# Optimization experiments

Measured on AMD Instinct MI355X. Metric: run time of the kernel, lower is better.

## Reference

```python
import jax, jax.numpy as jnp
import numpy as np

NUM_ITEMS = 50000
NUM_USERS = 16384   # static number of user segments (total_user universe)
H0 = 512            # encoder_hidden_size[0]
LAT = 256           # bottleneck (encoder_hidden_size[-1] / decoder_hidden_size[0])
N = 262144          # observed interactions
NT = 262144         # target interactions


def setup_inputs() -> dict:
    key = jax.random.key(0)
    ks = jax.random.split(key, 14)

    def glorot(k, shape):
        fan_in, fan_out = shape[1], shape[0]
        lim = np.sqrt(6.0 / (fan_in + fan_out)).astype(np.float32)
        return jax.random.uniform(k, shape, jnp.float32, -lim, lim)

    return {
        "user": jax.random.randint(ks[0], (N,), 0, NUM_USERS, jnp.int32),
        "item": jax.random.randint(ks[1], (N,), 0, NUM_ITEMS, jnp.int32),
        "rating": jax.random.normal(ks[2], (N,), jnp.float32),
        "target_user": jax.random.randint(ks[3], (NT,), 0, NUM_USERS, jnp.int32),
        "target_item": jax.random.randint(ks[4], (NT,), 0, NUM_ITEMS, jnp.int32),
        "target_rating": jax.random.normal(ks[5], (NT,), jnp.float32),
        # encoder_linear: Linear(num_items, H0)
        "W_enc": glorot(ks[6], (H0, NUM_ITEMS)),
        "b_enc": jnp.zeros((H0,), jnp.float32),
        # Encoder: Linear(H0, LAT) + Tanh
        "W1": glorot(ks[7], (LAT, H0)),
        "b1": jnp.zeros((LAT,), jnp.float32),
        # Decoder: Linear(LAT, H0) + Tanh
        "W2": glorot(ks[8], (H0, LAT)),
        "b2": jnp.zeros((H0,), jnp.float32),
        # decoder_linear: Linear(H0, num_items)
        "W_dec": glorot(ks[9], (NUM_ITEMS, H0)),
        "b_dec": jnp.zeros((NUM_ITEMS,), jnp.float32),
    }


def reference(user, item, rating, target_user, target_item, target_rating,
              W_enc, b_enc, W1, b1, W2, b2, W_dec, b_dec):
    # --- encoder: gather item weight rows, scale by rating, segment-sum per user ---
    # rows: [N, H0] gather from W_enc.T ([NUM_ITEMS, H0])
    rows = W_enc.T[item] * rating[:, None]
    # per-user aggregation over the full user universe (equivalent to the
    # torch unique/sort/index_add path: users with no interactions get 0 -> tanh(bias))
    agg = jax.ops.segment_sum(rows, user, num_segments=NUM_USERS)  # [U, H0]
    x = jnp.tanh(agg + b_enc)
    # --- small dense tanh MLP encoder/decoder ---
    encoded = jnp.tanh(x @ W1.T + b1)          # [U, LAT]
    decoded = jnp.tanh(encoded @ W2.T + b2)    # [U, H0] (dropout = identity, eval mode)
    # --- decoder: gather user codes & item decoder rows, rowwise dot ---
    g = decoded[target_user]                   # [NT, H0]
    w = W_dec[target_item]                     # [NT, H0]
    pred = jnp.sum(g * w, axis=-1) + b_dec[target_item]  # [NT]
    loss = jnp.mean((pred - target_rating) ** 2)
    return pred, loss
```

## Files before the change

kernel.cpp:

```cpp
#include <hip/hip_runtime.h>
#include <hip/hip_bf16.h>
#include <math.h>

#define NUM_ITEMS 50000
#define NUM_USERS 16384
#define ITEM_BINS 65536
#define H0 512
#define LAT 256
#define FP8_SCALE 64.0f
#define FP8_INV (1.0f / 64.0f)

typedef __attribute__((ext_vector_type(8))) short short8;
typedef __attribute__((ext_vector_type(4))) float floatx4;
typedef __attribute__((ext_vector_type(2))) float vf2;

__device__ __forceinline__ unsigned short f2bf(float f) {
    union { float f; unsigned i; } u; u.f = f;
    unsigned r = u.i + 0x7fff + ((u.i >> 16) & 1);
    return (unsigned short)(r >> 16);
}
__device__ __forceinline__ float bfhi(unsigned v) {
    union { unsigned i; float f; } u; u.i = v & 0xffff0000u; return u.f;
}
__device__ __forceinline__ float bflo(unsigned v) {
    union { unsigned i; float f; } u; u.i = v << 16; return u.f;
}
__device__ __forceinline__ uint4 pack8(const float* v) {
    uint4 p;
    p.x = (unsigned)f2bf(v[0]) | ((unsigned)f2bf(v[1]) << 16);
    p.y = (unsigned)f2bf(v[2]) | ((unsigned)f2bf(v[3]) << 16);
    p.z = (unsigned)f2bf(v[4]) | ((unsigned)f2bf(v[5]) << 16);
    p.w = (unsigned)f2bf(v[6]) | ((unsigned)f2bf(v[7]) << 16);
    return p;
}
__device__ __forceinline__ unsigned pkfp8_4(float a, float b, float c, float d) {
    int v = __builtin_amdgcn_cvt_pk_fp8_f32(a, b, 0, false);
    v = __builtin_amdgcn_cvt_pk_fp8_f32(c, d, v, true);
    return (unsigned)v;
}
__device__ __forceinline__ void fp8x4_to_f32(unsigned v, float* o) {
    vf2 lo = __builtin_amdgcn_cvt_pk_f32_fp8((int)v, false);
    vf2 hi = __builtin_amdgcn_cvt_pk_f32_fp8((int)v, true);
    o[0] = lo.x; o[1] = lo.y; o[2] = hi.x; o[3] = hi.y;
}

__global__ __launch_bounds__(256) void count_kernel(const int* __restrict__ user, int* __restrict__ cntU,
                                                    const int* __restrict__ t_item, int* __restrict__ cntI,
                                                    int n, int nt) {
    int i = (blockIdx.x * blockDim.x + threadIdx.x) * 4;
    if (i + 3 < n) {
        int4 u = *(const int4*)(user + i);
        atomicAdd(&cntU[u.x], 1); atomicAdd(&cntU[u.y], 1);
        atomicAdd(&cntU[u.z], 1); atomicAdd(&cntU[u.w], 1);
    } else {
        for (int k = i; k < n; ++k) atomicAdd(&cntU[user[k]], 1);
    }
    if (i + 3 < nt) {
        int4 t = *(const int4*)(t_item + i);
        atomicAdd(&cntI[t.x], 1); atomicAdd(&cntI[t.y], 1);
        atomicAdd(&cntI[t.z], 1); atomicAdd(&cntI[t.w], 1);
    } else {
        for (int k = i; k < nt; ++k) atomicAdd(&cntI[t_item[k]], 1);
    }
}

__device__ void scan_block(const int* __restrict__ cnt, int* __restrict__ offs,
                           int* __restrict__ cursor, int per) {
    __shared__ int ssum[1024];
    int t = threadIdx.x;
    int base = t * per;
    int s = 0;
    for (int j = 0; j < per; j += 4) {
        int4 v = *(const int4*)(cnt + base + j);
        s += v.x + v.y + v.z + v.w;
    }
    ssum[t] = s;
    __syncthreads();
    for (int off = 1; off < 1024; off <<= 1) {
        int v = (t >= off) ? ssum[t - off] : 0;
        __syncthreads();
        ssum[t] += v;
        __syncthreads();
    }
    int run = (t == 0) ? 0 : ssum[t - 1];
    for (int j = 0; j < per; j += 4) {
        int4 v = *(const int4*)(cnt + base + j);
        int4 o;
        o.x = run; run += v.x;
        o.y = run; run += v.y;
        o.z = run; run += v.z;
        o.w = run; run += v.w;
        *(int4*)(offs + base + j) = o;
        *(int4*)(cursor + base + j) = o;
    }
}

__global__ void scan_kernel(const int* __restrict__ cntU, int* __restrict__ offsU, int* __restrict__ curU,
                            const int* __restrict__ cntI, int* __restrict__ offsI, int* __restrict__ curI) {
    if (blockIdx.x == 0) scan_block(cntU, offsU, curU, NUM_USERS / 1024);
    else scan_block(cntI, offsI, curI, ITEM_BINS / 1024);
}

__global__ __launch_bounds__(256) void mega_kernel(
        const int* __restrict__ user, const int* __restrict__ item,
        const float* __restrict__ rating, int* __restrict__ curU, int2* __restrict__ s_pack,
        const int* __restrict__ t_user, const int* __restrict__ t_item,
        const float* __restrict__ t_rating, int* __restrict__ curI, int4* __restrict__ st_pack,
        const float* __restrict__ W_enc, unsigned char* __restrict__ wtb8,
        const float* __restrict__ W_dec, unsigned char* __restrict__ wdb8,
        const float* __restrict__ W1, unsigned short* __restrict__ w1b,
        const float* __restrict__ W2, unsigned short* __restrict__ w2b,
        int n, int nt, int SB, int TB, int DB) {
    __shared__ float tileT[64 * 129];
    int bid = blockIdx.x;
    int tid = threadIdx.x;
    if (bid < SB) {
        int i = bid * 256 + tid;
        if (i < n) {
            int u = user[i];
            int pos = atomicAdd(&curU[u], 1);
            s_pack[pos] = make_int2(item[i], __float_as_int(rating[i]));
        }
        if (i < nt) {
            int it = t_item[i];
            int pos = atomicAdd(&curI[it], 1);
            st_pack[pos] = make_int4(t_user[i], it, __float_as_int(t_rating[i]), i);
        }
    } else if (bid < SB + TB) {
        const int TBX = (NUM_ITEMS + 63) / 64;
        int b = bid - SB;
        int x0 = (b % TBX) * 64;
        int y0 = (b / TBX) * 128;
        int g = tid >> 4;
        int m = tid & 15;
        int ibase = m * 4;
#pragma unroll
        for (int p = 0; p < 8; ++p) {
            int hloc = p * 16 + g;
            int it = x0 + ibase;
            if (it < NUM_ITEMS) {
                float4 v = *(const float4*)(W_enc + (size_t)(y0 + hloc) * NUM_ITEMS + it);
                tileT[(ibase + 0) * 129 + hloc] = v.x;
                tileT[(ibase + 1) * 129 + hloc] = v.y;
                tileT[(ibase + 2) * 129 + hloc] = v.z;
                tileT[(ibase + 3) * 129 + hloc] = v.w;
            }
        }
        __syncthreads();
        int l = tid & 7;
        int i0 = tid >> 3;
#pragma unroll
        for (int p = 0; p < 2; ++p) {
            int i = p * 32 + i0;
            int it = x0 + i;
            if (it < NUM_ITEMS) {
                const float* src = tileT + i * 129 + l * 16;
                uint4 o;
                o.x = pkfp8_4(src[0] * FP8_SCALE, src[1] * FP8_SCALE, src[2] * FP8_SCALE, src[3] * FP8_SCALE);
                o.y = pkfp8_4(src[4] * FP8_SCALE, src[5] * FP8_SCALE, src[6] * FP8_SCALE, src[7] * FP8_SCALE);
                o.z = pkfp8_4(src[8] * FP8_SCALE, src[9] * FP8_SCALE, src[10] * FP8_SCALE, src[11] * FP8_SCALE);
                o.w = pkfp8_4(src[12] * FP8_SCALE, src[13] * FP8_SCALE, src[14] * FP8_SCALE, src[15] * FP8_SCALE);
                *(uint4*)(wtb8 + (size_t)it * H0 + y0 + l * 16) = o;
            }
        }
    } else if (bid < SB + TB + DB) {
        size_t idx = (size_t)(bid - SB - TB) * 4096 + tid * 16;
        float4 v0 = *(const float4*)(W_dec + idx);
        float4 v1 = *(const float4*)(W_dec + idx + 4);
        float4 v2 = *(const float4*)(W_dec + idx + 8);
        float4 v3 = *(const float4*)(W_dec + idx + 12);
        uint4 o;
        o.x = pkfp8_4(v0.x * FP8_SCALE, v0.y * FP8_SCALE, v0.z * FP8_SCALE, v0.w * FP8_SCALE);
        o.y = pkfp8_4(v1.x * FP8_SCALE, v1.y * FP8_SCALE, v1.z * FP8_SCALE, v1.w * FP8_SCALE);
        o.z = pkfp8_4(v2.x * FP8_SCALE, v2.y * FP8_SCALE, v2.z * FP8_SCALE, v2.w * FP8_SCALE);
        o.w = pkfp8_4(v3.x * FP8_SCALE, v3.y * FP8_SCALE, v3.z * FP8_SCALE, v3.w * FP8_SCALE);
        *(uint4*)(wdb8 + idx) = o;
    } else {
        int b2i = bid - SB - TB - DB;
        const float* src = (b2i < 64) ? W1 : W2;
        unsigned short* dst = (b2i < 64) ? w1b : w2b;
        int idx = (b2i & 63) * 2048 + tid * 8;
        float v[8];
        *(float4*)&v[0] = *(const float4*)(src + idx);
        *(float4*)&v[4] = *(const float4*)(src + idx + 4);
        *(uint4*)(dst + idx) = pack8(v);
    }
}

__global__ __launch_bounds__(256) void agg_kernel(const unsigned char* __restrict__ wtb8,
                                                  const int* __restrict__ offs,
                                                  const int* __restrict__ ends,
                                                  const int2* __restrict__ s_pack,
                                                  const float* __restrict__ b_enc,
                                                  unsigned short* __restrict__ xb) {
    __shared__ float red[3 * 512];
    int u = blockIdx.x;
    int tid = threadIdx.x;
    int g = tid >> 6, lane = tid & 63;
    float acc[8] = {};
    int j0 = offs[u], j1 = ends[u];
    int j = j0 + g;
    int2 nxt = (j < j1) ? s_pack[j] : make_int2(0, 0);
    while (j < j1) {
        int2 cur = nxt;
        int jn = j + 4;
        if (jn < j1) nxt = s_pack[jn];
        float r = __int_as_float(cur.y);
        uint2 v = ((const uint2*)(wtb8 + (size_t)cur.x * H0))[lane];
        float wf[8];
        fp8x4_to_f32(v.x, wf);
        fp8x4_to_f32(v.y, wf + 4);
#pragma unroll
        for (int e = 0; e < 8; ++e) acc[e] += wf[e] * r;
        j = jn;
    }
    if (g) {
        float4* rp = (float4*)red + (size_t)(g - 1) * 128 + lane * 2;
        rp[0] = make_float4(acc[0], acc[1], acc[2], acc[3]);
        rp[1] = make_float4(acc[4], acc[5], acc[6], acc[7]);
    }
    __syncthreads();
    if (g == 0) {
#pragma unroll
        for (int h = 0; h < 3; ++h) {
            const float* rp = red + h * 512 + lane * 8;
#pragma unroll
            for (int e = 0; e < 8; ++e) acc[e] += rp[e];
        }
        float4 b0 = ((const float4*)b_enc)[lane * 2];
        float4 b1 = ((const float4*)b_enc)[lane * 2 + 1];
        float o[8];
        o[0] = tanhf(acc[0] * FP8_INV + b0.x); o[1] = tanhf(acc[1] * FP8_INV + b0.y);
        o[2] = tanhf(acc[2] * FP8_INV + b0.z); o[3] = tanhf(acc[3] * FP8_INV + b0.w);
        o[4] = tanhf(acc[4] * FP8_INV + b1.x); o[5] = tanhf(acc[5] * FP8_INV + b1.y);
        o[6] = tanhf(acc[6] * FP8_INV + b1.z); o[7] = tanhf(acc[7] * FP8_INV + b1.w);
        ((uint4*)(xb + (size_t)u * H0))[lane] = pack8(o);
    }
}

template<int BN>
__global__ __launch_bounds__(256) void gemm_mfma(const unsigned short* __restrict__ A,
                                                 const unsigned short* __restrict__ B,
                                                 const float* __restrict__ bias,
                                                 unsigned short* __restrict__ C,
                                                 int Nn, int K) {
    constexpr int WN = BN / 32;
    constexpr int NCH = 8 + BN / 16;
    constexpr int PER = NCH / 4;
    __shared__ unsigned short Ash[128 * 32];
    __shared__ unsigned short Bsh[BN * 32];
    int tid = threadIdx.x;
    int wid = tid >> 6, lane = tid & 63;
    int wave_m = wid & 1, wave_n = wid >> 1;
    int quad = lane >> 4, l16 = lane & 15;
    int m0 = blockIdx.x * 128, n0 = blockIdx.y * BN;
    floatx4 acc[4][WN] = {};
    int srow = lane >> 2;
    int scol = (lane & 3) * 8;
    for (int k0 = 0; k0 < K; k0 += 32) {
#pragma unroll
        for (int i = 0; i < PER; ++i) {
            int c = wid * PER + i;
            if (c < 8) {
                const unsigned short* ga = A + (size_t)(m0 + c * 16 + srow) * K + k0 + scol;
                __builtin_amdgcn_global_load_lds(
                    (const __attribute__((address_space(1))) void*)ga,
                    (__attribute__((address_space(3))) void*)((__attribute__((address_space(3))) char*)Ash + c * 1024),
                    16, 0, 0);
            } else {
                const unsigned short* gb = B + (size_t)(n0 + (c - 8) * 16 + srow) * K + k0 + scol;
                __builtin_amdgcn_global_load_lds(
                    (const __attribute__((address_space(1))) void*)gb,
                    (__attribute__((address_space(3))) void*)((__attribute__((address_space(3))) char*)Bsh + (c - 8) * 1024),
                    16, 0, 0);
            }
        }
        __syncthreads();
        short8 af[4], bfr[WN];
#pragma unroll
        for (int i = 0; i < 4; ++i) {
            int ml = wave_m * 64 + i * 16 + l16;
            af[i] = ((const short8*)Ash)[ml * 4 + quad];
        }
#pragma unroll
        for (int j = 0; j < WN; ++j) {
            int nl = wave_n * (BN / 2) + j * 16 + l16;
            bfr[j] = ((const short8*)Bsh)[nl * 4 + quad];
        }
#pragma unroll
        for (int i = 0; i < 4; ++i)
#pragma unroll
            for (int j = 0; j < WN; ++j)
                acc[i][j] = __builtin_amdgcn_mfma_f32_16x16x32_bf16(af[i], bfr[j], acc[i][j], 0, 0, 0);
        __syncthreads();
    }
#pragma unroll
    for (int j = 0; j < WN; ++j) {
        int col = n0 + wave_n * (BN / 2) + j * 16 + l16;
        float bv = bias[col];
#pragma unroll
        for (int i = 0; i < 4; ++i) {
            int rowb = m0 + wave_m * 64 + i * 16 + quad * 4;
#pragma unroll
            for (int r = 0; r < 4; ++r)
                C[(size_t)(rowb + r) * Nn + col] = f2bf(tanhf(acc[i][j][r] + bv));
        }
    }
}

__global__ __launch_bounds__(256) void predict_kernel(const unsigned short* __restrict__ dec_b,
                                                      const unsigned char* __restrict__ wdb8,
                                                      const float* __restrict__ b_dec,
                                                      const int4* __restrict__ st,
                                                      float* __restrict__ pred,
                                                      float* __restrict__ partials, int NT) {
    __shared__ float wsum[4];
    int wid = threadIdx.x >> 6, lane = threadIdx.x & 63;
    int base = (blockIdx.x * 4 + wid) * 4;
    float sq = 0.f;
    int4 tv[4];
    uint4 gv[4];
    uint2 wv[4];
#pragma unroll
    for (int t = 0; t < 4; ++t) tv[t] = st[min(base + t, NT - 1)];
#pragma unroll
    for (int t = 0; t < 4; ++t) {
        gv[t] = ((const uint4*)(dec_b + (size_t)tv[t].x * H0))[lane];
        wv[t] = ((const uint2*)(wdb8 + (size_t)tv[t].y * H0))[lane];
    }
#pragma unroll
    for (int t = 0; t < 4; ++t) {
        float wf[8];
        fp8x4_to_f32(wv[t].x, wf);
        fp8x4_to_f32(wv[t].y, wf + 4);
        float s = bflo(gv[t].x) * wf[0] + bfhi(gv[t].x) * wf[1]
                + bflo(gv[t].y) * wf[2] + bfhi(gv[t].y) * wf[3]
                + bflo(gv[t].z) * wf[4] + bfhi(gv[t].z) * wf[5]
                + bflo(gv[t].w) * wf[6] + bfhi(gv[t].w) * wf[7];
#pragma unroll
        for (int off = 32; off; off >>= 1) s += __shfl_xor(s, off, 64);
        if (lane == 0 && base + t < NT) {
            float p = s * FP8_INV + b_dec[tv[t].y];
            pred[tv[t].w] = p;
            float d = p - __int_as_float(tv[t].z);
            sq += d * d;
        }
    }
    if (lane == 0) wsum[wid] = sq;
    __syncthreads();
    if (threadIdx.x == 0) partials[blockIdx.x] = wsum[0] + wsum[1] + wsum[2] + wsum[3];
}

__global__ void loss_reduce(const float* __restrict__ partials, float* __restrict__ out_loss,
                            int nPart, float invNT) {
    __shared__ float s[256];
    int t = threadIdx.x;
    float a = 0.f;
    const float4* p4 = (const float4*)partials;
    int n4 = nPart >> 2;
    for (int i = t; i < n4; i += 256) {
        float4 v = p4[i];
        a += v.x + v.y + v.z + v.w;
    }
    for (int i = (n4 << 2) + t; i < nPart; i += 256) a += partials[i];
    s[t] = a;
    __syncthreads();
    for (int off = 128; off; off >>= 1) {
        if (t < off) s[t] += s[t + off];
        __syncthreads();
    }
    if (t == 0) out_loss[0] = s[0] * invNT;
}

extern "C" void kernel_launch(void* const* d_in, const int* in_sizes, int n_in,
                              void* d_out, int out_size, void* d_ws, size_t ws_size,
                              hipStream_t stream) {
    const int* user = (const int*)d_in[0];
    const int* item = (const int*)d_in[1];
    const float* rating = (const float*)d_in[2];
    const int* t_user = (const int*)d_in[3];
    const int* t_item = (const int*)d_in[4];
    const float* t_rating = (const float*)d_in[5];
    const float* W_enc = (const float*)d_in[6];
    const float* b_enc = (const float*)d_in[7];
    const float* W1 = (const float*)d_in[8];
    const float* b1 = (const float*)d_in[9];
    const float* W2 = (const float*)d_in[10];
    const float* b2 = (const float*)d_in[11];
    const float* W_dec = (const float*)d_in[12];
    const float* b_dec = (const float*)d_in[13];
    const int N = in_sizes[0];
    const int NT = in_sizes[3];

    char* ws = (char*)d_ws;
    size_t off = 0;
    auto alloc = [&](size_t bytes) {
        void* p = ws + off;
        off = (off + bytes + 255) & ~(size_t)255;
        return p;
    };
    unsigned char* wtb8 = (unsigned char*)alloc((size_t)NUM_ITEMS * H0);
    unsigned char* wdb8 = (unsigned char*)alloc((size_t)NUM_ITEMS * H0);
    unsigned short* xb = (unsigned short*)alloc((size_t)NUM_USERS * H0 * 2);
    unsigned short* enc_b = (unsigned short*)alloc((size_t)NUM_USERS * LAT * 2);
    unsigned short* dec_b = (unsigned short*)alloc((size_t)NUM_USERS * H0 * 2);
    unsigned short* w1b = (unsigned short*)alloc((size_t)LAT * H0 * 2);
    unsigned short* w2b = (unsigned short*)alloc((size_t)H0 * LAT * 2);
    int* cntU = (int*)alloc((size_t)(NUM_USERS + ITEM_BINS) * 4);
    int* cntI = cntU + NUM_USERS;
    int* offsU = (int*)alloc((size_t)NUM_USERS * 4);
    int* curU = (int*)alloc((size_t)NUM_USERS * 4);
    int* offsI = (int*)alloc((size_t)ITEM_BINS * 4);
    int* curI = (int*)alloc((size_t)ITEM_BINS * 4);
    int2* s_pack = (int2*)alloc((size_t)N * 8);
    int4* st_pack = (int4*)alloc((size_t)NT * 16);
    const int predBlocks = (NT + 15) / 16;
    float* partials = (float*)alloc((size_t)predBlocks * 4);

    float* pred = (float*)d_out;
    float* loss = pred + NT;

    const int maxNNT = N > NT ? N : NT;
    const int SB = (maxNNT + 255) / 256;
    const int TBX = (NUM_ITEMS + 63) / 64;
    const int TB = TBX * (H0 / 128);
    const int DB = (NUM_ITEMS * H0) / 4096;
    const int WB = 128;

    hipMemsetAsync(cntU, 0, (size_t)(NUM_USERS + ITEM_BINS) * 4, stream);
    count_kernel<<<(maxNNT + 1023) / 1024, 256, 0, stream>>>(user, cntU, t_item, cntI, N, NT);
    scan_kernel<<<2, 1024, 0, stream>>>(cntU, offsU, curU, cntI, offsI, curI);
    mega_kernel<<<SB + TB + DB + WB, 256, 0, stream>>>(
        user, item, rating, curU, s_pack,
        t_user, t_item, t_rating, curI, st_pack,
        W_enc, wtb8, W_dec, wdb8, W1, w1b, W2, w2b,
        N, NT, SB, TB, DB);
    agg_kernel<<<NUM_USERS, 256, 0, stream>>>(wtb8, offsU, curU, s_pack, b_enc, xb);
    gemm_mfma<64><<<dim3(NUM_USERS / 128, LAT / 64), 256, 0, stream>>>(xb, w1b, b1, enc_b, LAT, H0);
    gemm_mfma<64><<<dim3(NUM_USERS / 128, H0 / 64), 256, 0, stream>>>(enc_b, w2b, b2, dec_b, H0, LAT);
    predict_kernel<<<predBlocks, 256, 0, stream>>>(dec_b, wdb8, b_dec, st_pack, pred, partials, NT);
    loss_reduce<<<1, 256, 0, stream>>>(partials, loss, predBlocks, 1.0f / NT);
}
```

Before: 450.9 us.

## Fuse encoder/decoder GEMMs, use one wave per user in aggregation, simplify conversions

```diff
diff --git a/kernel.cpp b/kernel.cpp
--- a/kernel.cpp
+++ b/kernel.cpp
@@ -9,6 +9,7 @@
 #define LAT 256
 #define FP8_SCALE 64.0f
 #define FP8_INV (1.0f / 64.0f)
+#define EPITCH 264
 
 typedef __attribute__((ext_vector_type(8))) short short8;
 typedef __attribute__((ext_vector_type(4))) float floatx4;
@@ -46,7 +47,8 @@
 
 __global__ __launch_bounds__(256) void count_kernel(const int* __restrict__ user, int* __restrict__ cntU,
                                                     const int* __restrict__ t_item, int* __restrict__ cntI,
-                                                    int n, int nt) {
+                                                    float* __restrict__ loss, int n, int nt) {
+    if (blockIdx.x == 0 && threadIdx.x == 0) loss[0] = 0.f;
     int i = (blockIdx.x * blockDim.x + threadIdx.x) * 4;
     if (i + 3 < n) {
         int4 u = *(const int4*)(user + i);
@@ -111,9 +113,9 @@
         const float* __restrict__ W1, unsigned short* __restrict__ w1b,
         const float* __restrict__ W2, unsigned short* __restrict__ w2b,
         int n, int nt, int SB, int TB, int DB) {
-    __shared__ float tileT[64 * 129];
     int bid = blockIdx.x;
     int tid = threadIdx.x;
+    int wid = tid >> 6, lane = tid & 63;
     if (bid < SB) {
         int i = bid * 256 + tid;
         if (i < n) {
@@ -130,60 +132,42 @@
         const int TBX = (NUM_ITEMS + 63) / 64;
         int b = bid - SB;
         int x0 = (b % TBX) * 64;
-        int y0 = (b / TBX) * 128;
-        int g = tid >> 4;
-        int m = tid & 15;
-        int ibase = m * 4;
-#pragma unroll
-        for (int p = 0; p < 8; ++p) {
-            int hloc = p * 16 + g;
-            int it = x0 + ibase;
-            if (it < NUM_ITEMS) {
-                float4 v = *(const float4*)(W_enc + (size_t)(y0 + hloc) * NUM_ITEMS + it);
-                tileT[(ibase + 0) * 129 + hloc] = v.x;
-                tileT[(ibase + 1) * 129 + hloc] = v.y;
-                tileT[(ibase + 2) * 129 + hloc] = v.z;
-                tileT[(ibase + 3) * 129 + hloc] = v.w;
-            }
-        }
-        __syncthreads();
-        int l = tid & 7;
-        int i0 = tid >> 3;
-#pragma unroll
-        for (int p = 0; p < 2; ++p) {
-            int i = p * 32 + i0;
-            int it = x0 + i;
-            if (it < NUM_ITEMS) {
-                const float* src = tileT + i * 129 + l * 16;
-                uint4 o;
-                o.x = pkfp8_4(src[0] * FP8_SCALE, src[1] * FP8_SCALE, src[2] * FP8_SCALE, src[3] * FP8_SCALE);
-                o.y = pkfp8_4(src[4] * FP8_SCALE, src[5] * FP8_SCALE, src[6] * FP8_SCALE, src[7] * FP8_SCALE);
-                o.z = pkfp8_4(src[8] * FP8_SCALE, src[9] * FP8_SCALE, src[10] * FP8_SCALE, src[11] * FP8_SCALE);
-                o.w = pkfp8_4(src[12] * FP8_SCALE, src[13] * FP8_SCALE, src[14] * FP8_SCALE, src[15] * FP8_SCALE);
-                *(uint4*)(wtb8 + (size_t)it * H0 + y0 + l * 16) = o;
-            }
+        int y0 = (b / TBX) * 64;
+        int h0 = y0 + wid * 16;
+        int it = x0 + lane;
+        if (it < NUM_ITEMS) {
+            float v[16];
+#pragma unroll
+            for (int e = 0; e < 16; ++e)
+                v[e] = W_enc[(size_t)(h0 + e) * NUM_ITEMS + it];
+            uint4 o;
+            o.x = pkfp8_4(v[0] * FP8_SCALE, v[1] * FP8_SCALE, v[2] * FP8_SCALE, v[3] * FP8_SCALE);
+            o.y = pkfp8_4(v[4] * FP8_SCALE, v[5] * FP8_SCALE, v[6] * FP8_SCALE, v[7] * FP8_SCALE);
+            o.z = pkfp8_4(v[8] * FP8_SCALE, v[9] * FP8_SCALE, v[10] * FP8_SCALE, v[11] * FP8_SCALE);
+            o.w = pkfp8_4(v[12] * FP8_SCALE, v[13] * FP8_SCALE, v[14] * FP8_SCALE, v[15] * FP8_SCALE);
+            *(uint4*)(wtb8 + (size_t)it * H0 + h0) = o;
         }
     } else if (bid < SB + TB + DB) {
-        size_t idx = (size_t)(bid - SB - TB) * 4096 + tid * 16;
-        float4 v0 = *(const float4*)(W_dec + idx);
-        float4 v1 = *(const float4*)(W_dec + idx + 4);
-        float4 v2 = *(const float4*)(W_dec + idx + 8);
-        float4 v3 = *(const float4*)(W_dec + idx + 12);
-        uint4 o;
-        o.x = pkfp8_4(v0.x * FP8_SCALE, v0.y * FP8_SCALE, v0.z * FP8_SCALE, v0.w * FP8_SCALE);
-        o.y = pkfp8_4(v1.x * FP8_SCALE, v1.y * FP8_SCALE, v1.z * FP8_SCALE, v1.w * FP8_SCALE);
-        o.z = pkfp8_4(v2.x * FP8_SCALE, v2.y * FP8_SCALE, v2.z * FP8_SCALE, v2.w * FP8_SCALE);
-        o.w = pkfp8_4(v3.x * FP8_SCALE, v3.y * FP8_SCALE, v3.z * FP8_SCALE, v3.w * FP8_SCALE);
-        *(uint4*)(wdb8 + idx) = o;
+        size_t base = (size_t)(bid - SB - TB) * 4096 + wid * 1024 + lane * 4;
+#pragma unroll
+        for (int c = 0; c < 4; ++c) {
+            float4 v = *(const float4*)(W_dec + base + c * 256);
+            *(unsigned*)(wdb8 + base + c * 256) =
+                pkfp8_4(v.x * FP8_SCALE, v.y * FP8_SCALE, v.z * FP8_SCALE, v.w * FP8_SCALE);
+        }
     } else {
         int b2i = bid - SB - TB - DB;
-        const float* src = (b2i < 64) ? W1 : W2;
-        unsigned short* dst = (b2i < 64) ? w1b : w2b;
-        int idx = (b2i & 63) * 2048 + tid * 8;
-        float v[8];
-        *(float4*)&v[0] = *(const float4*)(src + idx);
-        *(float4*)&v[4] = *(const float4*)(src + idx + 4);
-        *(uint4*)(dst + idx) = pack8(v);
+        const float* src = (b2i < 32) ? W1 : W2;
+        unsigned short* dst = (b2i < 32) ? w1b : w2b;
+        size_t base = (size_t)(b2i & 31) * 4096 + wid * 1024 + lane * 4;
+#pragma unroll
+        for (int c = 0; c < 4; ++c) {
+            float4 v = *(const float4*)(src + base + c * 256);
+            uint2 o;
+            o.x = (unsigned)f2bf(v.x) | ((unsigned)f2bf(v.y) << 16);
+            o.y = (unsigned)f2bf(v.z) | ((unsigned)f2bf(v.w) << 16);
+            *(uint2*)(dst + base + c * 256) = o;
+        }
     }
 }
 
@@ -193,117 +177,148 @@
                                                   const int2* __restrict__ s_pack,
                                                   const float* __restrict__ b_enc,
                                                   unsigned short* __restrict__ xb) {
-    __shared__ float red[3 * 512];
-    int u = blockIdx.x;
-    int tid = threadIdx.x;
-    int g = tid >> 6, lane = tid & 63;
+    int wid = threadIdx.x >> 6, lane = threadIdx.x & 63;
+    int u = blockIdx.x * 4 + wid;
+    int j0 = offs[u], j1 = ends[u];
     float acc[8] = {};
-    int j0 = offs[u], j1 = ends[u];
-    int j = j0 + g;
-    int2 nxt = (j < j1) ? s_pack[j] : make_int2(0, 0);
-    while (j < j1) {
-        int2 cur = nxt;
-        int jn = j + 4;
-        if (jn < j1) nxt = s_pack[jn];
-        float r = __int_as_float(cur.y);
-        uint2 v = ((const uint2*)(wtb8 + (size_t)cur.x * H0))[lane];
-        float wf[8];
-        fp8x4_to_f32(v.x, wf);
-        fp8x4_to_f32(v.y, wf + 4);
-#pragma unroll
-        for (int e = 0; e < 8; ++e) acc[e] += wf[e] * r;
-        j = jn;
-    }
-    if (g) {
-        float4* rp = (float4*)red + (size_t)(g - 1) * 128 + lane * 2;
-        rp[0] = make_float4(acc[0], acc[1], acc[2], acc[3]);
-        rp[1] = make_float4(acc[4], acc[5], acc[6], acc[7]);
-    }
-    __syncthreads();
-    if (g == 0) {
-#pragma unroll
-        for (int h = 0; h < 3; ++h) {
-            const float* rp = red + h * 512 + lane * 8;
-#pragma unroll
-            for (int e = 0; e < 8; ++e) acc[e] += rp[e];
-        }
-        float4 b0 = ((const float4*)b_enc)[lane * 2];
-        float4 b1 = ((const float4*)b_enc)[lane * 2 + 1];
-        float o[8];
-        o[0] = tanhf(acc[0] * FP8_INV + b0.x); o[1] = tanhf(acc[1] * FP8_INV + b0.y);
-        o[2] = tanhf(acc[2] * FP8_INV + b0.z); o[3] = tanhf(acc[3] * FP8_INV + b0.w);
-        o[4] = tanhf(acc[4] * FP8_INV + b1.x); o[5] = tanhf(acc[5] * FP8_INV + b1.y);
-        o[6] = tanhf(acc[6] * FP8_INV + b1.z); o[7] = tanhf(acc[7] * FP8_INV + b1.w);
-        ((uint4*)(xb + (size_t)u * H0))[lane] = pack8(o);
-    }
-}
-
-template<int BN>
-__global__ __launch_bounds__(256) void gemm_mfma(const unsigned short* __restrict__ A,
-                                                 const unsigned short* __restrict__ B,
-                                                 const float* __restrict__ bias,
-                                                 unsigned short* __restrict__ C,
-                                                 int Nn, int K) {
-    constexpr int WN = BN / 32;
-    constexpr int NCH = 8 + BN / 16;
-    constexpr int PER = NCH / 4;
-    __shared__ unsigned short Ash[128 * 32];
-    __shared__ unsigned short Bsh[BN * 32];
+    int j = j0;
+    for (; j + 1 < j1; j += 2) {
+        int2 a = s_pack[j];
+        int2 b = s_pack[j + 1];
+        uint2 va = ((const uint2*)(wtb8 + (size_t)a.x * H0))[lane];
+        uint2 vb = ((const uint2*)(wtb8 + (size_t)b.x * H0))[lane];
+        float ra = __int_as_float(a.y), rb = __int_as_float(b.y);
+        float wa[8], wb[8];
+        fp8x4_to_f32(va.x, wa); fp8x4_to_f32(va.y, wa + 4);
+        fp8x4_to_f32(vb.x, wb); fp8x4_to_f32(vb.y, wb + 4);
+#pragma unroll
+        for (int e = 0; e < 8; ++e) acc[e] += wa[e] * ra + wb[e] * rb;
+    }
+    if (j < j1) {
+        int2 a = s_pack[j];
+        uint2 va = ((const uint2*)(wtb8 + (size_t)a.x * H0))[lane];
+        float ra = __int_as_float(a.y);
+        float wa[8];
+        fp8x4_to_f32(va.x, wa); fp8x4_to_f32(va.y, wa + 4);
+#pragma unroll
+        for (int e = 0; e < 8; ++e) acc[e] += wa[e] * ra;
+    }
+    float4 b0 = ((const float4*)b_enc)[lane * 2];
+    float4 b1 = ((const float4*)b_enc)[lane * 2 + 1];
+    float o[8];
+    o[0] = tanhf(acc[0] * FP8_INV + b0.x); o[1] = tanhf(acc[1] * FP8_INV + b0.y);
+    o[2] = tanhf(acc[2] * FP8_INV + b0.z); o[3] = tanhf(acc[3] * FP8_INV + b0.w);
+    o[4] = tanhf(acc[4] * FP8_INV + b1.x); o[5] = tanhf(acc[5] * FP8_INV + b1.y);
+    o[6] = tanhf(acc[6] * FP8_INV + b1.z); o[7] = tanhf(acc[7] * FP8_INV + b1.w);
+    ((uint4*)(xb + (size_t)u * H0))[lane] = pack8(o);
+}
+
+__global__ __launch_bounds__(256) void mlp_kernel(const unsigned short* __restrict__ xb,
+                                                  const unsigned short* __restrict__ w1b,
+                                                  const float* __restrict__ b1,
+                                                  const unsigned short* __restrict__ w2b,
+                                                  const float* __restrict__ b2,
+                                                  unsigned short* __restrict__ dec_b) {
+    __shared__ unsigned short Ash[64 * 32];
+    __shared__ unsigned short Bsh[512 * 32];
+    __shared__ unsigned short encs[64 * EPITCH];
     int tid = threadIdx.x;
     int wid = tid >> 6, lane = tid & 63;
-    int wave_m = wid & 1, wave_n = wid >> 1;
     int quad = lane >> 4, l16 = lane & 15;
-    int m0 = blockIdx.x * 128, n0 = blockIdx.y * BN;
-    floatx4 acc[4][WN] = {};
+    int m0 = blockIdx.x * 64;
     int srow = lane >> 2;
     int scol = (lane & 3) * 8;
-    for (int k0 = 0; k0 < K; k0 += 32) {
-#pragma unroll
-        for (int i = 0; i < PER; ++i) {
-            int c = wid * PER + i;
-            if (c < 8) {
-                const unsigned short* ga = A + (size_t)(m0 + c * 16 + srow) * K + k0 + scol;
-                __builtin_amdgcn_global_load_lds(
-                    (const __attribute__((address_space(1))) void*)ga,
-                    (__attribute__((address_space(3))) void*)((__attribute__((address_space(3))) char*)Ash + c * 1024),
-                    16, 0, 0);
-            } else {
-                const unsigned short* gb = B + (size_t)(n0 + (c - 8) * 16 + srow) * K + k0 + scol;
-                __builtin_amdgcn_global_load_lds(
-                    (const __attribute__((address_space(1))) void*)gb,
-                    (__attribute__((address_space(3))) void*)((__attribute__((address_space(3))) char*)Bsh + (c - 8) * 1024),
-                    16, 0, 0);
+
+    {
+        floatx4 acc[4][4] = {};
+        for (int k0 = 0; k0 < 512; k0 += 32) {
+#pragma unroll
+            for (int i = 0; i < 5; ++i) {
+                int c = wid * 5 + i;
+                if (c < 4) {
+                    const unsigned short* ga = xb + (size_t)(m0 + c * 16 + srow) * 512 + k0 + scol;
+                    __builtin_amdgcn_global_load_lds(
+                        (const __attribute__((address_space(1))) void*)ga,
+                        (__attribute__((address_space(3))) void*)((__attribute__((address_space(3))) char*)Ash + c * 1024),
+                        16, 0, 0);
+                } else {
+                    const unsigned short* gb = w1b + (size_t)((c - 4) * 16 + srow) * 512 + k0 + scol;
+                    __builtin_amdgcn_global_load_lds(
+                        (const __attribute__((address_space(1))) void*)gb,
+                        (__attribute__((address_space(3))) void*)((__attribute__((address_space(3))) char*)Bsh + (c - 4) * 1024),
+                        16, 0, 0);
+                }
             }
+            __syncthreads();
+            short8 af[4], bfr[4];
+#pragma unroll
+            for (int i = 0; i < 4; ++i)
+                af[i] = ((const short8*)Ash)[(i * 16 + l16) * 4 + quad];
+#pragma unroll
+            for (int j = 0; j < 4; ++j) {
+                int nl = wid * 64 + j * 16 + l16;
+                bfr[j] = ((const short8*)Bsh)[nl * 4 + quad];
+            }
+#pragma unroll
+            for (int i = 0; i < 4; ++i)
+#pragma unroll
+                for (int j = 0; j < 4; ++j)
+                    acc[i][j] = __builtin_amdgcn_mfma_f32_16x16x32_bf16(af[i], bfr[j], acc[i][j], 0, 0, 0);
+            __syncthreads();
+        }
+#pragma unroll
+        for (int j = 0; j < 4; ++j) {
+            int col = wid * 64 + j * 16 + l16;
+            float bv = b1[col];
+#pragma unroll
+            for (int i = 0; i < 4; ++i) {
+                int row = i * 16 + quad * 4;
+#pragma unroll
+                for (int r = 0; r < 4; ++r)
+                    encs[(row + r) * EPITCH + col] = f2bf(tanhf(acc[i][j][r] + bv));
+            }
+        }
+    }
+    __syncthreads();
+
+    floatx4 acc2[4][8] = {};
+    for (int k0 = 0; k0 < 256; k0 += 32) {
+#pragma unroll
+        for (int i = 0; i < 8; ++i) {
+            int c = wid * 8 + i;
+            const unsigned short* gb = w2b + (size_t)(c * 16 + srow) * 256 + k0 + scol;
+            __builtin_amdgcn_global_load_lds(
+                (const __attribute__((address_space(1))) void*)gb,
+                (__attribute__((address_space(3))) void*)((__attribute__((address_space(3))) char*)Bsh + c * 1024),
+                16, 0, 0);
         }
         __syncthreads();
-        short8 af[4], bfr[WN];
+        short8 af[4], bfr[8];
+#pragma unroll
+        for (int i = 0; i < 4; ++i)
+            af[i] = *(const short8*)(encs + (size_t)(i * 16 + l16) * EPITCH + k0 + quad * 8);
+#pragma unroll
+        for (int j = 0; j < 8; ++j) {
+            int nl = wid * 128 + j * 16 + l16;
+            bfr[j] = ((const short8*)Bsh)[nl * 4 + quad];
+        }
+#pragma unroll
+        for (int i = 0; i < 4; ++i)
+#pragma unroll
+            for (int j = 0; j < 8; ++j)
+                acc2[i][j] = __builtin_amdgcn_mfma_f32_16x16x32_bf16(af[i], bfr[j], acc2[i][j], 0, 0, 0);
+        __syncthreads();
+    }
+#pragma unroll
+    for (int j = 0; j < 8; ++j) {
+        int col = wid * 128 + j * 16 + l16;
+        float bv = b2[col];
 #pragma unroll
         for (int i = 0; i < 4; ++i) {
-            int ml = wave_m * 64 + i * 16 + l16;
-            af[i] = ((const short8*)Ash)[ml * 4 + quad];
-        }
-#pragma unroll
-        for (int j = 0; j < WN; ++j) {
-            int nl = wave_n * (BN / 2) + j * 16 + l16;
-            bfr[j] = ((const short8*)Bsh)[nl * 4 + quad];
-        }
-#pragma unroll
-        for (int i = 0; i < 4; ++i)
-#pragma unroll
-            for (int j = 0; j < WN; ++j)
-                acc[i][j] = __builtin_amdgcn_mfma_f32_16x16x32_bf16(af[i], bfr[j], acc[i][j], 0, 0, 0);
-        __syncthreads();
-    }
-#pragma unroll
-    for (int j = 0; j < WN; ++j) {
-        int col = n0 + wave_n * (BN / 2) + j * 16 + l16;
-        float bv = bias[col];
-#pragma unroll
-        for (int i = 0; i < 4; ++i) {
-            int rowb = m0 + wave_m * 64 + i * 16 + quad * 4;
+            int row = m0 + i * 16 + quad * 4;
 #pragma unroll
             for (int r = 0; r < 4; ++r)
-                C[(size_t)(rowb + r) * Nn + col] = f2bf(tanhf(acc[i][j][r] + bv));
+                dec_b[(size_t)(row + r) * 512 + col] = f2bf(tanhf(acc2[i][j][r] + bv));
         }
     }
 }
@@ -402,7 +417,6 @@
     unsigned char* wtb8 = (unsigned char*)alloc((size_t)NUM_ITEMS * H0);
     unsigned char* wdb8 = (unsigned char*)alloc((size_t)NUM_ITEMS * H0);
     unsigned short* xb = (unsigned short*)alloc((size_t)NUM_USERS * H0 * 2);
-    unsigned short* enc_b = (unsigned short*)alloc((size_t)NUM_USERS * LAT * 2);
     unsigned short* dec_b = (unsigned short*)alloc((size_t)NUM_USERS * H0 * 2);
     unsigned short* w1b = (unsigned short*)alloc((size_t)LAT * H0 * 2);
     unsigned short* w2b = (unsigned short*)alloc((size_t)H0 * LAT * 2);
@@ -423,21 +437,20 @@
     const int maxNNT = N > NT ? N : NT;
     const int SB = (maxNNT + 255) / 256;
     const int TBX = (NUM_ITEMS + 63) / 64;
-    const int TB = TBX * (H0 / 128);
+    const int TB = TBX * (H0 / 64);
     const int DB = (NUM_ITEMS * H0) / 4096;
-    const int WB = 128;
+    const int WB = 64;
 
     hipMemsetAsync(cntU, 0, (size_t)(NUM_USERS + ITEM_BINS) * 4, stream);
-    count_kernel<<<(maxNNT + 1023) / 1024, 256, 0, stream>>>(user, cntU, t_item, cntI, N, NT);
+    count_kernel<<<(maxNNT + 1023) / 1024, 256, 0, stream>>>(user, cntU, t_item, cntI, loss, N, NT);
     scan_kernel<<<2, 1024, 0, stream>>>(cntU, offsU, curU, cntI, offsI, curI);
     mega_kernel<<<SB + TB + DB + WB, 256, 0, stream>>>(
         user, item, rating, curU, s_pack,
         t_user, t_item, t_rating, curI, st_pack,
         W_enc, wtb8, W_dec, wdb8, W1, w1b, W2, w2b,
         N, NT, SB, TB, DB);
-    agg_kernel<<<NUM_USERS, 256, 0, stream>>>(wtb8, offsU, curU, s_pack, b_enc, xb);
-    gemm_mfma<64><<<dim3(NUM_USERS / 128, LAT / 64), 256, 0, stream>>>(xb, w1b, b1, enc_b, LAT, H0);
-    gemm_mfma<64><<<dim3(NUM_USERS / 128, H0 / 64), 256, 0, stream>>>(enc_b, w2b, b2, dec_b, H0, LAT);
+    agg_kernel<<<NUM_USERS / 4, 256, 0, stream>>>(wtb8, offsU, curU, s_pack, b_enc, xb);
+    mlp_kernel<<<NUM_USERS / 64, 256, 0, stream>>>(xb, w1b, b1, w2b, b2, dec_b);
     predict_kernel<<<predBlocks, 256, 0, stream>>>(dec_b, wdb8, b_dec, st_pack, pred, partials, NT);
     loss_reduce<<<1, 256, 0, stream>>>(partials, loss, predBlocks, 1.0f / NT);
 }
```

Result: slower. 463.3 us (+2.7%).
